# Kernel tuning notes

Hardware: AMD Instinct MI355X
Metric: run time of the kernel (lower is better)

Reference implementation:

```python
import jax, jax.numpy as jnp
import numpy as np

B, D, H = 524288, 64, 19  # batch, input_size, hidden_size


def setup_inputs() -> dict:
    key = jax.random.key(0)
    ks = jax.random.split(key, 4)
    x = jax.random.normal(ks[0], (B, D), dtype=jnp.float32)
    # nn.Linear params (stored as [out, in] like torch)
    Wi = jax.random.normal(ks[1], (H, D), dtype=jnp.float32) / np.sqrt(D).astype(np.float32)
    bi = jnp.zeros((H,), jnp.float32)
    Wr = jax.random.normal(ks[2], (H, H), dtype=jnp.float32) / np.sqrt(H).astype(np.float32)
    Wo = jax.random.normal(ks[3], (H, H), dtype=jnp.float32) / np.sqrt(H).astype(np.float32)
    bo = jnp.zeros((H,), jnp.float32)
    tau = jnp.full((H,), 0.5, jnp.float32)        # nn.Parameter(ones*0.5)
    tau_adapt = jnp.full((H,), 0.1, jnp.float32)  # nn.Parameter(ones*0.1)
    return {"x": x, "Wi": Wi, "bi": bi, "Wr": Wr, "Wo": Wo, "bo": bo,
            "tau": tau, "tau_adapt": tau_adapt, "steps": 10}


def reference(x, Wi, bi, Wr, Wo, bo, tau, tau_adapt, steps):
    dt = 0.01
    # scalar urgency over the whole input, clamped from below
    urgency = jnp.maximum(jnp.abs(x).mean(), 0.01)
    tau_dyn = jnp.clip(tau * (1.0 - tau_adapt) + tau_adapt / urgency, 0.01, 10.0)  # [H]
    mapped = x @ Wi.T + bi  # [B, H], computed once outside the loop
    h0 = jnp.zeros((x.shape[0], tau.shape[0]), x.dtype)

    def step(h, _):
        act = jnp.tanh(mapped + h @ Wr.T)
        h = h + dt * ((-h + act) / tau_dyn)
        return h, None

    h, _ = jax.lax.scan(step, h0, None, length=steps)
    return (h @ Wo.T + bo, h)
```

## Files before the change

kernel.cpp:

```cpp
#include <hip/hip_runtime.h>

#define NB 524288
#define ND 64
#define NH 19

__device__ __forceinline__ float fast_tanh(float x) {
    x = fminf(9.0f, fmaxf(-9.0f, x));
    float e = __expf(2.0f * x);
    return 1.0f - 2.0f * __builtin_amdgcn_rcpf(e + 1.0f);
}

#define ROWS_A 2
extern "C" __global__ void __launch_bounds__(256)
ltc_mapped_urgency(const float* __restrict__ x, const float* __restrict__ Wi,
                   const float* __restrict__ bi, float* __restrict__ mapped,
                   double* __restrict__ acc)
{
    const int gid = blockIdx.x * 256 + threadIdx.x;
    const int T = NB / ROWS_A;
    float m[ROWS_A][NH];
#pragma unroll
    for (int r = 0; r < ROWS_A; ++r)
#pragma unroll
        for (int j = 0; j < NH; ++j) m[r][j] = bi[j];
    float s = 0.f;
#pragma unroll
    for (int q = 0; q < ND / 4; ++q) {
        float4 v[ROWS_A];
#pragma unroll
        for (int r = 0; r < ROWS_A; ++r) {
            v[r] = ((const float4*)(x + (size_t)(gid + r * T) * ND))[q];
            s += fabsf(v[r].x) + fabsf(v[r].y) + fabsf(v[r].z) + fabsf(v[r].w);
        }
#pragma unroll
        for (int j = 0; j < NH; ++j) {
            const float w0 = Wi[j * ND + 4 * q + 0];
            const float w1 = Wi[j * ND + 4 * q + 1];
            const float w2 = Wi[j * ND + 4 * q + 2];
            const float w3 = Wi[j * ND + 4 * q + 3];
#pragma unroll
            for (int r = 0; r < ROWS_A; ++r) {
                m[r][j] = fmaf(v[r].x, w0, m[r][j]);
                m[r][j] = fmaf(v[r].y, w1, m[r][j]);
                m[r][j] = fmaf(v[r].z, w2, m[r][j]);
                m[r][j] = fmaf(v[r].w, w3, m[r][j]);
            }
        }
    }
#pragma unroll
    for (int r = 0; r < ROWS_A; ++r)
#pragma unroll
        for (int j = 0; j < NH; ++j)
            mapped[(size_t)j * NB + (gid + r * T)] = m[r][j];
#pragma unroll
    for (int off = 32; off > 0; off >>= 1) s += __shfl_down(s, off, 64);
    __shared__ float red[4];
    const int lane = threadIdx.x & 63, w = threadIdx.x >> 6;
    if (lane == 0) red[w] = s;
    __syncthreads();
    if (threadIdx.x == 0) atomicAdd(acc, (double)(red[0] + red[1] + red[2] + red[3]));
}

__global__ void __launch_bounds__(256)
ltc_steps(const float* __restrict__ mapped, const double* __restrict__ acc,
          const float* __restrict__ Wr, const float* __restrict__ Wo,
          const float* __restrict__ bo, const float* __restrict__ tau,
          const float* __restrict__ ta, const int* __restrict__ steps_p,
          float* __restrict__ out)
{
    const int t = threadIdx.x;
    const int b = blockIdx.x * 256 + t;
    const double mean = *acc * (1.0 / ((double)NB * (double)ND));
    const float u = fmaxf((float)mean, 0.01f);
    float rr[NH];
#pragma unroll
    for (int j = 0; j < NH; ++j) {
        float td = tau[j] * (1.f - ta[j]) + ta[j] / u;
        td = fminf(10.f, fmaxf(0.01f, td));
        rr[j] = 0.01f / td;
    }
    float m[NH], h[NH];
#pragma unroll
    for (int j = 0; j < NH; ++j) {
        m[j] = mapped[(size_t)j * NB + b];
        h[j] = 0.f;
    }
    const int steps = *steps_p;
    for (int s = 0; s < steps; ++s) {
        float a[NH];
#pragma unroll
        for (int j = 0; j < NH; ++j) {
            float p = m[j];
#pragma unroll
            for (int k = 0; k < NH; ++k)
                p = fmaf(h[k], Wr[j * NH + k], p);
            a[j] = fast_tanh(p);
        }
#pragma unroll
        for (int j = 0; j < NH; ++j) h[j] = fmaf(rr[j], a[j] - h[j], h[j]);
    }
    __shared__ float st[256 * NH];
#pragma unroll
    for (int j = 0; j < NH; ++j) {
        float p = bo[j];
#pragma unroll
        for (int k = 0; k < NH; ++k) p = fmaf(h[k], Wo[j * NH + k], p);
        st[t * NH + j] = p;
    }
    __syncthreads();
    {
        const float4* s4 = (const float4*)st;
        float4* o4 = (float4*)(out + (size_t)blockIdx.x * 256 * NH);
#pragma unroll
        for (int i = 0; i < (256 * NH) / (4 * 256); ++i)
            o4[t + i * 256] = s4[t + i * 256];
        if (t + 1024 < 1216) o4[t + 1024] = s4[t + 1024];
    }
    __syncthreads();
#pragma unroll
    for (int j = 0; j < NH; ++j) st[t * NH + j] = h[j];
    __syncthreads();
    {
        const float4* s4 = (const float4*)st;
        float4* o4 = (float4*)(out + (size_t)NB * NH + (size_t)blockIdx.x * 256 * NH);
#pragma unroll
        for (int i = 0; i < (256 * NH) / (4 * 256); ++i)
            o4[t + i * 256] = s4[t + i * 256];
        if (t + 1024 < 1216) o4[t + 1024] = s4[t + 1024];
    }
}

extern "C" void kernel_launch(void* const* d_in, const int* in_sizes, int n_in,
                              void* d_out, int out_size, void* d_ws, size_t ws_size,
                              hipStream_t stream)
{
    const float* x   = (const float*)d_in[0];
    const float* Wi  = (const float*)d_in[1];
    const float* bi  = (const float*)d_in[2];
    const float* Wr  = (const float*)d_in[3];
    const float* Wo  = (const float*)d_in[4];
    const float* bo  = (const float*)d_in[5];
    const float* tau = (const float*)d_in[6];
    const float* ta  = (const float*)d_in[7];
    const int* steps = (const int*)d_in[8];
    float* out = (float*)d_out;

    double* acc = (double*)d_ws;
    float* mapped = (float*)((char*)d_ws + 16);

    hipMemsetAsync(d_ws, 0, sizeof(double), stream);
    ltc_mapped_urgency<<<NB / ROWS_A / 256, 256, 0, stream>>>(x, Wi, bi, mapped, acc);
    ltc_steps<<<NB / 256, 256, 0, stream>>>(mapped, acc, Wr, Wo, bo, tau, ta, steps, out);
}
```

Before: 409.9 us.

## Use packed float2 FMAs, rational tanh, LDS-staged input and partial-sum reduction

Rewrites both kernels. The recurrent and output matmuls are repacked into float2-paired weights so packed FMA instructions can process two hidden units at once. Exp-based tanh is replaced with a clamped Padé rational approximation. The first kernel stages x through LDS for coalesced loads. The double atomic plus memset is replaced by per-block partial sums that every block of the second kernel reduces redundantly. Costs are an extra setup launch, a slight accuracy change from the tanh approximation, and a 8192-element partial read per block.

Measured after the change: 357.6 us. 1.15x faster.

```diff
diff --git a/kernel.cpp b/kernel.cpp
--- a/kernel.cpp
+++ b/kernel.cpp
@@ -3,129 +3,187 @@
 #define NB 524288
 #define ND 64
 #define NH 19
-
-__device__ __forceinline__ float fast_tanh(float x) {
-    x = fminf(9.0f, fmaxf(-9.0f, x));
-    float e = __expf(2.0f * x);
-    return 1.0f - 2.0f * __builtin_amdgcn_rcpf(e + 1.0f);
-}
-
-#define ROWS_A 2
+#define NP 10
+#define NBLK_A 8192
+
+typedef float v2f __attribute__((ext_vector_type(2)));
+
+__device__ __forceinline__ v2f splat2(float x) { return (v2f){x, x}; }
+__device__ __forceinline__ v2f fma2(v2f a, v2f b, v2f c) {
+    return __builtin_elementwise_fma(a, b, c);
+}
+
+__device__ __forceinline__ v2f tanh2(v2f x) {
+    v2f x2 = x * x;
+    v2f n  = fma2(x2, x2 + splat2(105.f), splat2(945.f));
+    v2f d  = fma2(x2, fma2(x2, splat2(15.f), splat2(420.f)), splat2(945.f));
+    v2f xn = x * n;
+    v2f y  = {xn.x * __builtin_amdgcn_rcpf(d.x), xn.y * __builtin_amdgcn_rcpf(d.y)};
+    y = __builtin_elementwise_min(y, splat2(1.f));
+    y = __builtin_elementwise_max(y, splat2(-1.f));
+    return y;
+}
+
+extern "C" __global__ void __launch_bounds__(64)
+ltc_setup(const float* __restrict__ Wr, const float* __restrict__ Wo,
+          const float* __restrict__ bo, float2* __restrict__ Wr2,
+          float2* __restrict__ Wo2, float2* __restrict__ bo2)
+{
+    for (int i = threadIdx.x; i < NH * NP; i += 64) {
+        int k = i / NP, t = i % NP;
+        float rx = Wr[(2 * t) * NH + k];
+        float ry = (2 * t + 1 < NH) ? Wr[(2 * t + 1) * NH + k] : 0.f;
+        Wr2[i] = make_float2(rx, ry);
+        float ox = Wo[(2 * t) * NH + k];
+        float oy = (2 * t + 1 < NH) ? Wo[(2 * t + 1) * NH + k] : 0.f;
+        Wo2[i] = make_float2(ox, oy);
+    }
+    if (threadIdx.x < NP) {
+        int t = threadIdx.x;
+        bo2[t] = make_float2(bo[2 * t], (2 * t + 1 < NH) ? bo[2 * t + 1] : 0.f);
+    }
+}
+
+extern "C" __global__ void __launch_bounds__(64)
+ltc_a(const float* __restrict__ x, const float* __restrict__ Wi,
+      const float* __restrict__ bi, float* __restrict__ mapped,
+      float* __restrict__ partials)
+{
+    __shared__ float tile[64 * 66];
+    const int l = threadIdx.x;
+    const int rowbase = blockIdx.x * 64;
+    const float4* xg = (const float4*)x + (size_t)rowbase * (ND / 4);
+    float s = 0.f;
+#pragma unroll
+    for (int i = 0; i < 16; ++i) {
+        const float4 v = xg[i * 64 + l];
+        s += fabsf(v.x) + fabsf(v.y) + fabsf(v.z) + fabsf(v.w);
+        const int f = i * 64 + l, row = f >> 4, c = f & 15;
+        *(float2*)&tile[row * 66 + c * 4]     = make_float2(v.x, v.y);
+        *(float2*)&tile[row * 66 + c * 4 + 2] = make_float2(v.z, v.w);
+    }
+    __syncthreads();
+    float m[NH];
+#pragma unroll
+    for (int j = 0; j < NH; ++j) m[j] = bi[j];
+#pragma unroll
+    for (int q = 0; q < ND / 2; ++q) {
+        const float2 v = *(const float2*)&tile[l * 66 + 2 * q];
+#pragma unroll
+        for (int j = 0; j < NH; ++j) {
+            m[j] = fmaf(v.x, Wi[j * ND + 2 * q], m[j]);
+            m[j] = fmaf(v.y, Wi[j * ND + 2 * q + 1], m[j]);
+        }
+    }
+#pragma unroll
+    for (int j = 0; j < NH; ++j) mapped[(size_t)j * NB + rowbase + l] = m[j];
+#pragma unroll
+    for (int off = 32; off > 0; off >>= 1) s += __shfl_down(s, off, 64);
+    if (l == 0) partials[blockIdx.x] = s;
+}
+
 extern "C" __global__ void __launch_bounds__(256)
-ltc_mapped_urgency(const float* __restrict__ x, const float* __restrict__ Wi,
-                   const float* __restrict__ bi, float* __restrict__ mapped,
-                   double* __restrict__ acc)
-{
-    const int gid = blockIdx.x * 256 + threadIdx.x;
-    const int T = NB / ROWS_A;
-    float m[ROWS_A][NH];
-#pragma unroll
-    for (int r = 0; r < ROWS_A; ++r)
-#pragma unroll
-        for (int j = 0; j < NH; ++j) m[r][j] = bi[j];
-    float s = 0.f;
-#pragma unroll
-    for (int q = 0; q < ND / 4; ++q) {
-        float4 v[ROWS_A];
-#pragma unroll
-        for (int r = 0; r < ROWS_A; ++r) {
-            v[r] = ((const float4*)(x + (size_t)(gid + r * T) * ND))[q];
-            s += fabsf(v[r].x) + fabsf(v[r].y) + fabsf(v[r].z) + fabsf(v[r].w);
-        }
-#pragma unroll
-        for (int j = 0; j < NH; ++j) {
-            const float w0 = Wi[j * ND + 4 * q + 0];
-            const float w1 = Wi[j * ND + 4 * q + 1];
-            const float w2 = Wi[j * ND + 4 * q + 2];
-            const float w3 = Wi[j * ND + 4 * q + 3];
-#pragma unroll
-            for (int r = 0; r < ROWS_A; ++r) {
-                m[r][j] = fmaf(v[r].x, w0, m[r][j]);
-                m[r][j] = fmaf(v[r].y, w1, m[r][j]);
-                m[r][j] = fmaf(v[r].z, w2, m[r][j]);
-                m[r][j] = fmaf(v[r].w, w3, m[r][j]);
-            }
-        }
-    }
-#pragma unroll
-    for (int r = 0; r < ROWS_A; ++r)
-#pragma unroll
-        for (int j = 0; j < NH; ++j)
-            mapped[(size_t)j * NB + (gid + r * T)] = m[r][j];
-#pragma unroll
-    for (int off = 32; off > 0; off >>= 1) s += __shfl_down(s, off, 64);
+ltc_b(const float* __restrict__ mapped, const float* __restrict__ partials,
+      const float2* __restrict__ Wr2, const float2* __restrict__ Wo2,
+      const float2* __restrict__ bo2, const float* __restrict__ tau,
+      const float* __restrict__ ta, const int* __restrict__ steps_p,
+      float* __restrict__ out)
+{
+    __shared__ float st[256 * NH];
     __shared__ float red[4];
-    const int lane = threadIdx.x & 63, w = threadIdx.x >> 6;
-    if (lane == 0) red[w] = s;
-    __syncthreads();
-    if (threadIdx.x == 0) atomicAdd(acc, (double)(red[0] + red[1] + red[2] + red[3]));
-}
-
-__global__ void __launch_bounds__(256)
-ltc_steps(const float* __restrict__ mapped, const double* __restrict__ acc,
-          const float* __restrict__ Wr, const float* __restrict__ Wo,
-          const float* __restrict__ bo, const float* __restrict__ tau,
-          const float* __restrict__ ta, const int* __restrict__ steps_p,
-          float* __restrict__ out)
-{
     const int t = threadIdx.x;
     const int b = blockIdx.x * 256 + t;
-    const double mean = *acc * (1.0 / ((double)NB * (double)ND));
-    const float u = fmaxf((float)mean, 0.01f);
-    float rr[NH];
-#pragma unroll
-    for (int j = 0; j < NH; ++j) {
-        float td = tau[j] * (1.f - ta[j]) + ta[j] / u;
-        td = fminf(10.f, fmaxf(0.01f, td));
-        rr[j] = 0.01f / td;
-    }
-    float m[NH], h[NH];
-#pragma unroll
-    for (int j = 0; j < NH; ++j) {
-        m[j] = mapped[(size_t)j * NB + b];
-        h[j] = 0.f;
-    }
+
+    float ps = 0.f;
+#pragma unroll
+    for (int i = 0; i < NBLK_A / 256; ++i) ps += partials[t + 256 * i];
+#pragma unroll
+    for (int off = 32; off > 0; off >>= 1) ps += __shfl_down(ps, off, 64);
+    if ((t & 63) == 0) red[t >> 6] = ps;
+    __syncthreads();
+    const float total = red[0] + red[1] + red[2] + red[3];
+    const float u = fmaxf(total * (1.f / ((float)NB * (float)ND)), 0.01f);
+    const float inv_u = 1.f / u;
+
+    v2f rr2[NP];
+#pragma unroll
+    for (int j = 0; j < NP; ++j) {
+        int j0 = 2 * j, j1 = (2 * j + 1 < NH) ? 2 * j + 1 : 2 * j;
+        float t0 = fminf(10.f, fmaxf(0.01f, tau[j0] * (1.f - ta[j0]) + ta[j0] * inv_u));
+        float t1 = fminf(10.f, fmaxf(0.01f, tau[j1] * (1.f - ta[j1]) + ta[j1] * inv_u));
+        rr2[j] = (v2f){0.01f / t0, 0.01f / t1};
+    }
+
+    v2f m2[NP], h2[NP];
+#pragma unroll
+    for (int j = 0; j < NP - 1; ++j)
+        m2[j] = (v2f){mapped[(size_t)(2 * j) * NB + b],
+                      mapped[(size_t)(2 * j + 1) * NB + b]};
+    m2[NP - 1] = (v2f){mapped[(size_t)(NH - 1) * NB + b], 0.f};
+#pragma unroll
+    for (int j = 0; j < NP; ++j) h2[j] = splat2(0.f);
+
     const int steps = *steps_p;
+    const v2f* wr = (const v2f*)Wr2;
     for (int s = 0; s < steps; ++s) {
-        float a[NH];
-#pragma unroll
-        for (int j = 0; j < NH; ++j) {
-            float p = m[j];
-#pragma unroll
-            for (int k = 0; k < NH; ++k)
-                p = fmaf(h[k], Wr[j * NH + k], p);
-            a[j] = fast_tanh(p);
+        v2f p2[NP];
+        {
+            const v2f hb = splat2(h2[0].x);
+#pragma unroll
+            for (int j = 0; j < NP; ++j) p2[j] = fma2(hb, wr[j], m2[j]);
         }
 #pragma unroll
-        for (int j = 0; j < NH; ++j) h[j] = fmaf(rr[j], a[j] - h[j], h[j]);
-    }
-    __shared__ float st[256 * NH];
-#pragma unroll
-    for (int j = 0; j < NH; ++j) {
-        float p = bo[j];
-#pragma unroll
-        for (int k = 0; k < NH; ++k) p = fmaf(h[k], Wo[j * NH + k], p);
-        st[t * NH + j] = p;
-    }
+        for (int k = 1; k < NH; ++k) {
+            const float hk = (k & 1) ? h2[k >> 1].y : h2[k >> 1].x;
+            const v2f hb = splat2(hk);
+            const v2f* wrow = wr + k * NP;
+#pragma unroll
+            for (int j = 0; j < NP; ++j) p2[j] = fma2(hb, wrow[j], p2[j]);
+        }
+#pragma unroll
+        for (int j = 0; j < NP; ++j) p2[j] = tanh2(p2[j]);
+#pragma unroll
+        for (int j = 0; j < NP; ++j) h2[j] = fma2(rr2[j], p2[j] - h2[j], h2[j]);
+    }
+
+    const v2f* wo = (const v2f*)Wo2;
+    v2f o2[NP];
+    {
+        const v2f hb = splat2(h2[0].x);
+        const v2f* bb = (const v2f*)bo2;
+#pragma unroll
+        for (int j = 0; j < NP; ++j) o2[j] = fma2(hb, wo[j], bb[j]);
+    }
+#pragma unroll
+    for (int k = 1; k < NH; ++k) {
+        const float hk = (k & 1) ? h2[k >> 1].y : h2[k >> 1].x;
+        const v2f hb = splat2(hk);
+        const v2f* worow = wo + k * NP;
+#pragma unroll
+        for (int j = 0; j < NP; ++j) o2[j] = fma2(hb, worow[j], o2[j]);
+    }
+    __syncthreads();
+#pragma unroll
+    for (int j = 0; j < NH; ++j)
+        st[t * NH + j] = (j & 1) ? o2[j >> 1].y : o2[j >> 1].x;
     __syncthreads();
     {
         const float4* s4 = (const float4*)st;
         float4* o4 = (float4*)(out + (size_t)blockIdx.x * 256 * NH);
 #pragma unroll
-        for (int i = 0; i < (256 * NH) / (4 * 256); ++i)
-            o4[t + i * 256] = s4[t + i * 256];
+        for (int i = 0; i < 4; ++i) o4[t + i * 256] = s4[t + i * 256];
         if (t + 1024 < 1216) o4[t + 1024] = s4[t + 1024];
     }
     __syncthreads();
 #pragma unroll
-    for (int j = 0; j < NH; ++j) st[t * NH + j] = h[j];
+    for (int j = 0; j < NH; ++j)
+        st[t * NH + j] = (j & 1) ? h2[j >> 1].y : h2[j >> 1].x;
     __syncthreads();
     {
         const float4* s4 = (const float4*)st;
         float4* o4 = (float4*)(out + (size_t)NB * NH + (size_t)blockIdx.x * 256 * NH);
 #pragma unroll
-        for (int i = 0; i < (256 * NH) / (4 * 256); ++i)
-            o4[t + i * 256] = s4[t + i * 256];
+        for (int i = 0; i < 4; ++i) o4[t + i * 256] = s4[t + i * 256];
         if (t + 1024 < 1216) o4[t + 1024] = s4[t + 1024];
     }
 }
@@ -145,10 +203,14 @@
     const int* steps = (const int*)d_in[8];
     float* out = (float*)d_out;
 
-    double* acc = (double*)d_ws;
-    float* mapped = (float*)((char*)d_ws + 16);
-
-    hipMemsetAsync(d_ws, 0, sizeof(double), stream);
-    ltc_mapped_urgency<<<NB / ROWS_A / 256, 256, 0, stream>>>(x, Wi, bi, mapped, acc);
-    ltc_steps<<<NB / 256, 256, 0, stream>>>(mapped, acc, Wr, Wo, bo, tau, ta, steps, out);
-}
+    float*  partials = (float*)d_ws;
+    float2* Wr2 = (float2*)((char*)d_ws + 32768);
+    float2* Wo2 = (float2*)((char*)d_ws + 34304);
+    float2* bo2 = (float2*)((char*)d_ws + 35840);
+    float*  mapped = (float*)((char*)d_ws + 36864);
+
+    ltc_setup<<<1, 64, 0, stream>>>(Wr, Wo, bo, Wr2, Wo2, bo2);
+    ltc_a<<<NBLK_A, 64, 0, stream>>>(x, Wi, bi, mapped, partials);
+    ltc_b<<<NB / 256, 256, 0, stream>>>(mapped, partials, Wr2, Wo2, bo2,
+                                        tau, ta, steps, out);
+}
```
